# Performance work log

Measured on AMD Instinct MI355X. Metric: run time of the kernel, lower is better.

The kernel has to match this reference:

```python
import jax, jax.numpy as jnp
import numpy as np

B, S, D = 2, 2048, 768
H = 12
HD = D // H  # 64
SCALE = HD ** -0.5


def setup_inputs() -> dict:
    key = jax.random.key(0)
    k1, k2, k3, k4, k5 = jax.random.split(key, 5)
    x = jax.random.normal(k1, (B, S, D), dtype=jnp.float32)
    w_qkv = jax.random.normal(k2, (D, 3 * D), dtype=jnp.float32) * (D ** -0.5)
    b_qkv = jax.random.normal(k3, (3 * D,), dtype=jnp.float32) * 0.02
    w_proj = jax.random.normal(k4, (D, D), dtype=jnp.float32) * (D ** -0.5)
    b_proj = jax.random.normal(k5, (D,), dtype=jnp.float32) * 0.02
    return {"x": x, "w_qkv": w_qkv, "b_qkv": b_qkv, "w_proj": w_proj, "b_proj": b_proj}


def reference(x, w_qkv, b_qkv, w_proj, b_proj):
    b, s, d = x.shape
    # QKV projection: (B,S,3D) -> (3,B,H,S,HD)
    qkv = x @ w_qkv + b_qkv
    qkv = qkv.reshape(b, s, 3, H, HD).transpose(2, 0, 3, 1, 4)
    q, k, v = qkv[0], qkv[1], qkv[2]
    q = q * SCALE
    # full NxN attention scores, as in the original module
    attn = jnp.einsum("bhqd,bhkd->bhqk", q, k)
    attn = jax.nn.softmax(attn, axis=-1)
    out = jnp.einsum("bhqk,bhkd->bhqd", attn, v)  # (B,H,S,HD)
    out = out.transpose(0, 2, 1, 3).reshape(b, s, d)
    return out @ w_proj + b_proj
```

## Files before the change

### kernel.cpp

```cpp
#include <hip/hip_runtime.h>
#include <hip/hip_bf16.h>

#define B_ 2
#define S_ 2048
#define D_ 768
#define H_ 12
#define HD_ 64
#define EXP2C_ 0.1803368801111244f

typedef __attribute__((ext_vector_type(8))) short bf16x8;
typedef __attribute__((ext_vector_type(8))) unsigned short u16x8;
typedef __attribute__((ext_vector_type(4))) float f32x4;
typedef __attribute__((ext_vector_type(4))) unsigned int u32x4;

static __device__ __forceinline__ unsigned short f2bf(float x) {
    union { float f; unsigned u; } v; v.f = x;
    unsigned r = (v.u + 0x7FFFu + ((v.u >> 16) & 1u)) >> 16;
    return (unsigned short)r;
}
static __device__ __forceinline__ float bf2f(unsigned short h) {
    union { unsigned u; float f; } v; v.u = ((unsigned)h) << 16;
    return v.f;
}
static __device__ __forceinline__ float fexp2(float x) { return __builtin_exp2f(x); }

static __device__ __forceinline__ unsigned pk_bf16(float a, float b) {
    __hip_bfloat162 pk = __float22bfloat162_rn(make_float2(a, b));
    union { __hip_bfloat162 h; unsigned u; } v; v.h = pk;
    return v.u;
}

static __device__ __forceinline__ f32x4 mfma32(bf16x8 a, bf16x8 b, f32x4 c) {
    return __builtin_amdgcn_mfma_f32_16x16x32_bf16(a, b, c, 0, 0, 0);
}

typedef __attribute__((address_space(3))) unsigned int lds_u32;
typedef __attribute__((address_space(1))) const unsigned int glb_u32;
static __device__ __forceinline__ void glds16(const unsigned short* g, unsigned short* l) {
    __builtin_amdgcn_global_load_lds((glb_u32*)g, (lds_u32*)l, 16, 0, 0);
}

#define PREP_CONV_ 1536
#define PREP_TQKV_ 1728
#define PREP_TPRJ_ 576
__global__ __launch_bounds__(256) void prep_kernel(
    const float* __restrict__ x,      unsigned short* __restrict__ x16,
    const float* __restrict__ w_qkv,  unsigned short* __restrict__ wqkvT,
    const float* __restrict__ w_proj, unsigned short* __restrict__ wprojT)
{
    __shared__ float tile[32][33];
    const int bid = blockIdx.x, t = threadIdx.x;
    if (bid < PREP_CONV_) {
        const int i = (bid * 256 + t) * 8;
        float4 a0 = *(const float4*)(x + i);
        float4 a1 = *(const float4*)(x + i + 4);
        u16x8 s;
        s[0] = f2bf(a0.x); s[1] = f2bf(a0.y); s[2] = f2bf(a0.z); s[3] = f2bf(a0.w);
        s[4] = f2bf(a1.x); s[5] = f2bf(a1.y); s[6] = f2bf(a1.z); s[7] = f2bf(a1.w);
        *(u16x8*)(x16 + i) = s;
        return;
    }
    const float* w; unsigned short* wT; int N, bb;
    if (bid < PREP_CONV_ + PREP_TQKV_) { w = w_qkv; wT = wqkvT; N = 3 * D_; bb = bid - PREP_CONV_; }
    else                               { w = w_proj; wT = wprojT; N = D_;   bb = bid - PREP_CONV_ - PREP_TQKV_; }
    const int K = D_;
    const int nt = N / 32;
    const int n0 = (bb % nt) * 32, k0 = (bb / nt) * 32;
    const int tx = t & 31, ty = t >> 5;
#pragma unroll
    for (int i = 0; i < 4; i++)
        tile[ty + i * 8][tx] = w[(size_t)(k0 + ty + i * 8) * N + n0 + tx];
    __syncthreads();
#pragma unroll
    for (int i = 0; i < 4; i++)
        wT[(size_t)(n0 + ty + i * 8) * K + k0 + tx] = f2bf(tile[tx][ty + i * 8]);
}

template <int BM, int BN, bool OUT_F32>
__global__ __launch_bounds__(256) void gemm_bt_kernel(
    const unsigned short* __restrict__ A,
    const unsigned short* __restrict__ Bt,
    const float* __restrict__ bias,
    void* __restrict__ Cp,
    int M, int N, int K)
{
    __shared__ __align__(16) unsigned short As[BM][32];
    __shared__ __align__(16) unsigned short Bs[BN][32];
    constexpr int MI = BM / 32, NJ = BN / 32;
    constexpr int ACH = BM * 4, BCH = BN * 4;

    const int t = threadIdx.x;
    const int w = t >> 6, lane = t & 63, quad = lane >> 4, l16 = lane & 15;
    const int n0 = blockIdx.x * BN, m0 = blockIdx.y * BM;
    const int mw = (w & 1) * (BM / 2), nw = (w >> 1) * (BN / 2);

    const f32x4 z = {0.f, 0.f, 0.f, 0.f};
    f32x4 acc[MI][NJ];
#pragma unroll
    for (int i = 0; i < MI; i++)
#pragma unroll
        for (int j = 0; j < NJ; j++) acc[i][j] = z;

    for (int kk = 0; kk < K; kk += 32) {
#pragma unroll
        for (int it = 0; it < (ACH + 255) / 256; it++) {
            const int c = t + it * 256;
            if (ACH % 256 == 0 || c < ACH) {
                const int row = c >> 2, c8 = (c & 3) << 3;
                glds16(A + (size_t)(m0 + row) * K + kk + c8, &As[0][0] + c * 8);
            }
        }
#pragma unroll
        for (int it = 0; it < (BCH + 255) / 256; it++) {
            const int c = t + it * 256;
            if (BCH % 256 == 0 || c < BCH) {
                const int row = c >> 2, c8 = (c & 3) << 3;
                glds16(Bt + (size_t)(n0 + row) * K + kk + c8, &Bs[0][0] + c * 8);
            }
        }
        __syncthreads();

        bf16x8 a[MI], b[NJ];
#pragma unroll
        for (int i = 0; i < MI; i++)
            a[i] = *(const bf16x8*)(&As[mw + i * 16 + l16][quad * 8]);
#pragma unroll
        for (int j = 0; j < NJ; j++)
            b[j] = *(const bf16x8*)(&Bs[nw + j * 16 + l16][quad * 8]);
#pragma unroll
        for (int i = 0; i < MI; i++)
#pragma unroll
            for (int j = 0; j < NJ; j++)
                acc[i][j] = mfma32(a[i], b[j], acc[i][j]);
        __syncthreads();
    }

#pragma unroll
    for (int j = 0; j < NJ; j++) {
        const int col = n0 + nw + j * 16 + l16;
        const float bv = bias[col];
#pragma unroll
        for (int i = 0; i < MI; i++) {
#pragma unroll
            for (int r = 0; r < 4; r++) {
                const int row = m0 + mw + i * 16 + quad * 4 + r;
                const float v = acc[i][j][r] + bv;
                if (OUT_F32) ((float*)Cp)[(size_t)row * N + col] = v;
                else         ((unsigned short*)Cp)[(size_t)row * N + col] = f2bf(v);
            }
        }
    }
}

__global__ __launch_bounds__(256) void repack_v_kernel(
    const unsigned short* __restrict__ qkv,
    unsigned short* __restrict__ vt)
{
    __shared__ unsigned short T[64][65];
    const int t = threadIdx.x;
    const int bh = blockIdx.x, st = blockIdx.y;
    const int b = bh / H_, h = bh % H_;
    const unsigned short* src =
        qkv + (size_t)(b * S_ + st * 64) * (3 * D_) + 2 * D_ + h * HD_;

#pragma unroll
    for (int it = 0; it < 2; it++) {
        const int c = t + it * 256, sr = c >> 3, g = c & 7;
        u16x8 v = *(const u16x8*)(src + (size_t)sr * (3 * D_) + g * 8);
#pragma unroll
        for (int j = 0; j < 8; j++) T[sr][g * 8 + j] = v[j];
    }
    __syncthreads();
#pragma unroll
    for (int it = 0; it < 2; it++) {
        const int c = t + it * 256, hd = c >> 3, g = c & 7;
        u16x8 v;
#pragma unroll
        for (int j = 0; j < 8; j++) v[j] = T[g * 8 + j][hd];
        *(u16x8*)(vt + (size_t)(bh * HD_ + hd) * S_ + st * 64 + g * 8) = v;
    }
}

__global__ __launch_bounds__(256) void attn_kernel(
    const unsigned short* __restrict__ qkv,
    const unsigned short* __restrict__ vt,
    unsigned short* __restrict__ o)
{
    __shared__ __align__(16) unsigned short Ks[2][64][64];
    __shared__ __align__(16) unsigned short Vs[2][64][64];

    const int t = threadIdx.x;
    const int w = t >> 6, lane = t & 63, quad = lane >> 4, l16 = lane & 15;
    const int h8 = l16 & 7;
    const int qt = blockIdx.x, bh = blockIdx.y;
    const int b = bh / H_, h = bh % H_;
    const int ld = 3 * D_;

    const unsigned short* qbase =
        qkv + (size_t)(b * S_ + qt * 64 + 16 * w + l16) * ld + h * HD_;
    u16x8 qr0 = *(const u16x8*)(qbase + quad * 8);
    u16x8 qr1 = *(const u16x8*)(qbase + 32 + quad * 8);
    bf16x8 qf0, qf1;
#pragma unroll
    for (int j = 0; j < 8; j++) {
        qf0[j] = (short)f2bf(bf2f(qr0[j]) * EXP2C_);
        qf1[j] = (short)f2bf(bf2f(qr1[j]) * EXP2C_);
    }

    bf16x8 ones;
#pragma unroll
    for (int j = 0; j < 8; j++) ones[j] = (short)0x3F80;

    const unsigned short* kbase = qkv + (size_t)(b * S_) * ld + D_ + h * HD_;
    const unsigned short* vbase = vt + (size_t)bh * HD_ * S_;

    const int c0 = t, c1 = t + 256;
    const int row0 = c0 >> 3, row1 = c1 >> 3;
    const int kg0 = (c0 & 7) ^ ((row0 & 3) | (((row0 >> 3) & 1) << 2));
    const int kg1 = (c1 & 7) ^ ((row1 & 3) | (((row1 >> 3) & 1) << 2));
    const int vg0 = (c0 & 7) ^ (row0 & 7);
    const int vg1 = (c1 & 7) ^ (row1 & 7);
    const unsigned short* kp0 = kbase + (size_t)row0 * ld + kg0 * 8;
    const unsigned short* kp1 = kbase + (size_t)row1 * ld + kg1 * 8;
    const unsigned short* vp0 = vbase + (size_t)row0 * S_ + vg0 * 8;
    const unsigned short* vp1 = vbase + (size_t)row1 * S_ + vg1 * 8;
    const size_t KSTEP = (size_t)64 * ld;

    const f32x4 z = {0.f, 0.f, 0.f, 0.f};
    f32x4 o_acc[4] = {z, z, z, z};
    f32x4 l_acc = z;

    glds16(kp0, &Ks[0][0][0] + c0 * 8);
    glds16(kp1, &Ks[0][0][0] + c1 * 8);
    glds16(vp0, &Vs[0][0][0] + c0 * 8);
    glds16(vp1, &Vs[0][0][0] + c1 * 8);
    kp0 += KSTEP; kp1 += KSTEP; vp0 += 64; vp1 += 64;
    __syncthreads();

    const int NT = S_ / 64;
    for (int kt = 0; kt < NT; kt++) {
        const int buf = kt & 1;

        if (kt + 1 < NT) {
            unsigned short* kd = &Ks[buf ^ 1][0][0];
            unsigned short* vd = &Vs[buf ^ 1][0][0];
            glds16(kp0, kd + c0 * 8);
            glds16(kp1, kd + c1 * 8);
            glds16(vp0, vd + c0 * 8);
            glds16(vp1, vd + c1 * 8);
            kp0 += KSTEP; kp1 += KSTEP; vp0 += 64; vp1 += 64;
        }

        f32x4 s_acc[4] = {z, z, z, z};
#pragma unroll
        for (int nt = 0; nt < 4; nt++) {
            const int rowp = ((nt >> 1) << 5) + ((l16 >> 2) << 3) + ((nt & 1) << 2) + (l16 & 3);
            const int skr = (rowp & 3) | (((rowp >> 3) & 1) << 2);
            const unsigned short* kr = &Ks[buf][rowp][0];
            bf16x8 k0 = *(const bf16x8*)(kr + (quad ^ skr) * 8);
            bf16x8 k1 = *(const bf16x8*)(kr + ((quad ^ skr) ^ 4) * 8);
            s_acc[nt] = mfma32(k0, qf0, s_acc[nt]);
            s_acc[nt] = mfma32(k1, qf1, s_acc[nt]);
        }

        bf16x8 vr0[4], vr1[4];
#pragma unroll
        for (int nt = 0; nt < 4; nt++) {
            const int row = nt * 16 + l16;
            vr0[nt] = *(const bf16x8*)(&Vs[buf][row][(quad ^ h8) * 8]);
            vr1[nt] = *(const bf16x8*)(&Vs[buf][row][((quad ^ h8) ^ 4) * 8]);
        }

        f32x4 pr[4];
#pragma unroll
        for (int nt = 0; nt < 4; nt++) {
#pragma unroll
            for (int r = 0; r < 4; r++) pr[nt][r] = fexp2(s_acc[nt][r]);
        }
        union { u32x4 u; bf16x8 h; } ca, cb;
        ca.u[0] = pk_bf16(pr[0][0], pr[0][1]);
        ca.u[1] = pk_bf16(pr[0][2], pr[0][3]);
        ca.u[2] = pk_bf16(pr[1][0], pr[1][1]);
        ca.u[3] = pk_bf16(pr[1][2], pr[1][3]);
        cb.u[0] = pk_bf16(pr[2][0], pr[2][1]);
        cb.u[1] = pk_bf16(pr[2][2], pr[2][3]);
        cb.u[2] = pk_bf16(pr[3][0], pr[3][1]);
        cb.u[3] = pk_bf16(pr[3][2], pr[3][3]);
        const bf16x8 pa0 = ca.h, pa1 = cb.h;

        l_acc = mfma32(pa0, ones, l_acc);
        l_acc = mfma32(pa1, ones, l_acc);

#pragma unroll
        for (int nt = 0; nt < 4; nt++) {
            o_acc[nt] = mfma32(pa0, vr0[nt], o_acc[nt]);
            o_acc[nt] = mfma32(pa1, vr1[nt], o_acc[nt]);
        }

        __syncthreads();
    }

#pragma unroll
    for (int r = 0; r < 4; r++) {
        const float inv = 1.f / l_acc[r];
        const int row = b * S_ + qt * 64 + 16 * w + quad * 4 + r;
        unsigned short* ob = o + (size_t)row * D_ + h * HD_;
#pragma unroll
        for (int nt = 0; nt < 4; nt++)
            ob[nt * 16 + l16] = f2bf(o_acc[nt][r] * inv);
    }
}

extern "C" void kernel_launch(void* const* d_in, const int* in_sizes, int n_in,
                              void* d_out, int out_size, void* d_ws, size_t ws_size,
                              hipStream_t stream) {
    const float* x      = (const float*)d_in[0];
    const float* w_qkv  = (const float*)d_in[1];
    const float* b_qkv  = (const float*)d_in[2];
    const float* w_proj = (const float*)d_in[3];
    const float* b_proj = (const float*)d_in[4];
    float* out = (float*)d_out;

    unsigned short* qkv    = (unsigned short*)d_ws;
    unsigned short* vtb    = qkv    + (size_t)(B_ * S_) * (3 * D_);
    unsigned short* o_x16  = vtb    + (size_t)(B_ * H_) * HD_ * S_;
    unsigned short* wqkvT  = o_x16  + (size_t)(B_ * S_) * D_;
    unsigned short* wprojT = wqkvT  + (size_t)D_ * (3 * D_);

    dim3 blk(256);
    prep_kernel<<<dim3(PREP_CONV_ + PREP_TQKV_ + PREP_TPRJ_), blk, 0, stream>>>(
        x, o_x16, w_qkv, wqkvT, w_proj, wprojT);
    gemm_bt_kernel<128, 96, false><<<dim3((3 * D_) / 96, (B_ * S_) / 128), blk, 0, stream>>>(
        o_x16, wqkvT, b_qkv, qkv, B_ * S_, 3 * D_, D_);
    repack_v_kernel<<<dim3(B_ * H_, S_ / 64), blk, 0, stream>>>(qkv, vtb);
    attn_kernel<<<dim3(S_ / 64, B_ * H_), blk, 0, stream>>>(qkv, vtb, o_x16);
    gemm_bt_kernel<64, 64, true><<<dim3(D_ / 64, (B_ * S_) / 64), blk, 0, stream>>>(
        o_x16, wprojT, b_proj, out, B_ * S_, D_, D_);
}
```

Baseline: 174.2 us.

## Split attention over two key halves with a separate combine kernel

The attention kernel now splits the key/value sequence into two halves through a third grid dimension, so twice as many blocks run. Each block writes unnormalized fp32 partial outputs and row sums. A new combine kernel adds the two halves, normalizes and converts to bf16 for the projection GEMM. This is meant to raise parallelism in the attention stage. In exchange it adds large fp32 partial writes and reads, plus an extra kernel launch, and it reuses the output buffer as scratch.

```diff
diff --git a/kernel.cpp b/kernel.cpp
--- a/kernel.cpp
+++ b/kernel.cpp
@@ -184,7 +184,9 @@
 __global__ __launch_bounds__(256) void attn_kernel(
     const unsigned short* __restrict__ qkv,
     const unsigned short* __restrict__ vt,
-    unsigned short* __restrict__ o)
+    float* __restrict__ o_p0,
+    float* __restrict__ o_p1,
+    float* __restrict__ l_p)
 {
     __shared__ __align__(16) unsigned short Ks[2][64][64];
     __shared__ __align__(16) unsigned short Vs[2][64][64];
@@ -192,7 +194,7 @@
     const int t = threadIdx.x;
     const int w = t >> 6, lane = t & 63, quad = lane >> 4, l16 = lane & 15;
     const int h8 = l16 & 7;
-    const int qt = blockIdx.x, bh = blockIdx.y;
+    const int qt = blockIdx.x, bh = blockIdx.y, ks = blockIdx.z;
     const int b = bh / H_, h = bh % H_;
     const int ld = 3 * D_;
 
@@ -211,7 +213,8 @@
 #pragma unroll
     for (int j = 0; j < 8; j++) ones[j] = (short)0x3F80;
 
-    const unsigned short* kbase = qkv + (size_t)(b * S_) * ld + D_ + h * HD_;
+    const unsigned short* kbase =
+        qkv + (size_t)(b * S_ + ks * 1024) * ld + D_ + h * HD_;
     const unsigned short* vbase = vt + (size_t)bh * HD_ * S_;
 
     const int c0 = t, c1 = t + 256;
@@ -222,8 +225,8 @@
     const int vg1 = (c1 & 7) ^ (row1 & 7);
     const unsigned short* kp0 = kbase + (size_t)row0 * ld + kg0 * 8;
     const unsigned short* kp1 = kbase + (size_t)row1 * ld + kg1 * 8;
-    const unsigned short* vp0 = vbase + (size_t)row0 * S_ + vg0 * 8;
-    const unsigned short* vp1 = vbase + (size_t)row1 * S_ + vg1 * 8;
+    const unsigned short* vp0 = vbase + (size_t)row0 * S_ + ks * 1024 + vg0 * 8;
+    const unsigned short* vp1 = vbase + (size_t)row1 * S_ + ks * 1024 + vg1 * 8;
     const size_t KSTEP = (size_t)64 * ld;
 
     const f32x4 z = {0.f, 0.f, 0.f, 0.f};
@@ -237,7 +240,7 @@
     kp0 += KSTEP; kp1 += KSTEP; vp0 += 64; vp1 += 64;
     __syncthreads();
 
-    const int NT = S_ / 64;
+    const int NT = 1024 / 64;
     for (int kt = 0; kt < NT; kt++) {
         const int buf = kt & 1;
 
@@ -300,15 +303,40 @@
         __syncthreads();
     }
 
+    float* op = ks ? o_p1 : o_p0;
+    float* lp2 = l_p + (size_t)ks * (B_ * S_ * H_);
 #pragma unroll
     for (int r = 0; r < 4; r++) {
-        const float inv = 1.f / l_acc[r];
         const int row = b * S_ + qt * 64 + 16 * w + quad * 4 + r;
-        unsigned short* ob = o + (size_t)row * D_ + h * HD_;
+        float* ob = op + (size_t)row * D_ + h * HD_;
 #pragma unroll
         for (int nt = 0; nt < 4; nt++)
-            ob[nt * 16 + l16] = f2bf(o_acc[nt][r] * inv);
-    }
+            ob[nt * 16 + l16] = o_acc[nt][r];
+        if (l16 == 0) lp2[(size_t)row * H_ + h] = l_acc[r];
+    }
+}
+
+__global__ __launch_bounds__(256) void combine_kernel(
+    const float* __restrict__ o_p0,
+    const float* __restrict__ o_p1,
+    const float* __restrict__ l_p,
+    unsigned short* __restrict__ o)
+{
+    const int i = (blockIdx.x * 256 + threadIdx.x) * 8;
+    const int row = i / D_, col = i - row * D_, h = col >> 6;
+    const float l0 = l_p[(size_t)row * H_ + h];
+    const float l1 = l_p[(size_t)(B_ * S_ * H_) + row * H_ + h];
+    const float inv = 1.f / (l0 + l1);
+    float4 a0 = *(const float4*)(o_p0 + i);
+    float4 a1 = *(const float4*)(o_p0 + i + 4);
+    float4 b0 = *(const float4*)(o_p1 + i);
+    float4 b1 = *(const float4*)(o_p1 + i + 4);
+    u16x8 s;
+    s[0] = f2bf((a0.x + b0.x) * inv); s[1] = f2bf((a0.y + b0.y) * inv);
+    s[2] = f2bf((a0.z + b0.z) * inv); s[3] = f2bf((a0.w + b0.w) * inv);
+    s[4] = f2bf((a1.x + b1.x) * inv); s[5] = f2bf((a1.y + b1.y) * inv);
+    s[6] = f2bf((a1.z + b1.z) * inv); s[7] = f2bf((a1.w + b1.w) * inv);
+    *(u16x8*)(o + i) = s;
 }
 
 extern "C" void kernel_launch(void* const* d_in, const int* in_sizes, int n_in,
@@ -326,6 +354,9 @@
     unsigned short* o_x16  = vtb    + (size_t)(B_ * H_) * HD_ * S_;
     unsigned short* wqkvT  = o_x16  + (size_t)(B_ * S_) * D_;
     unsigned short* wprojT = wqkvT  + (size_t)D_ * (3 * D_);
+    float* o_p1 = (float*)(wprojT + (size_t)D_ * D_);
+    float* l_p  = o_p1 + (size_t)(B_ * S_) * D_;
+    float* o_p0 = out;
 
     dim3 blk(256);
     prep_kernel<<<dim3(PREP_CONV_ + PREP_TQKV_ + PREP_TPRJ_), blk, 0, stream>>>(
@@ -333,7 +364,9 @@
     gemm_bt_kernel<128, 96, false><<<dim3((3 * D_) / 96, (B_ * S_) / 128), blk, 0, stream>>>(
         o_x16, wqkvT, b_qkv, qkv, B_ * S_, 3 * D_, D_);
     repack_v_kernel<<<dim3(B_ * H_, S_ / 64), blk, 0, stream>>>(qkv, vtb);
-    attn_kernel<<<dim3(S_ / 64, B_ * H_), blk, 0, stream>>>(qkv, vtb, o_x16);
+    attn_kernel<<<dim3(S_ / 64, B_ * H_, 2), blk, 0, stream>>>(qkv, vtb, o_p0, o_p1, l_p);
+    combine_kernel<<<dim3((B_ * S_) * D_ / (256 * 8)), blk, 0, stream>>>(
+        o_p0, o_p1, l_p, o_x16);
     gemm_bt_kernel<64, 64, true><<<dim3(D_ / 64, (B_ * S_) / 64), blk, 0, stream>>>(
         o_x16, wprojT, b_proj, out, B_ * S_, D_, D_);
 }
```

After: 176.3 us. Within noise of the previous version (+1.2%).
